# Kernel optimization log

Measured on AMD Instinct MI355X. Metric: run time of the kernel, lower is better.

The kernel has to match this reference:

```python
import jax, jax.numpy as jnp
import numpy as np

N_NODES = 50000
N_EDGES = 800000
IN_FEAT = 128
N_HEADS = 4
OUT_FEAT = 16
NEG_SLOPE = 0.2


def setup_inputs() -> dict:
    key = jax.random.key(0)
    k1, k2, k3, k4, k5 = jax.random.split(key, 5)
    x = jax.random.normal(k1, (N_NODES, IN_FEAT), dtype=jnp.float32)
    src = jax.random.randint(k2, (N_EDGES,), 0, N_NODES)
    dst = jax.random.randint(k3, (N_EDGES,), 0, N_NODES)
    edge_index = jnp.stack([src, dst]).astype(jnp.int64)
    # xavier-uniform-like init for params
    limW = np.sqrt(6.0 / (IN_FEAT + N_HEADS * OUT_FEAT))
    W = jax.random.uniform(k4, (IN_FEAT, N_HEADS * OUT_FEAT), minval=-limW, maxval=limW, dtype=jnp.float32)
    lima = np.sqrt(6.0 / (N_HEADS + 2 * OUT_FEAT))
    a = jax.random.uniform(k5, (1, N_HEADS, 2 * OUT_FEAT), minval=-lima, maxval=lima, dtype=jnp.float32)
    return {"x": x, "edge_index": edge_index, "W": W, "a": a}


def reference(x, edge_index, W, a):
    N = x.shape[0]
    H = a.shape[1]
    F = a.shape[2] // 2
    src, dst = edge_index[0], edge_index[1]
    # node projection: [N, H, F]
    h = (x @ W).reshape(N, H, F)
    # split attention vector: sum(a * cat(h_src, h_dst)) = a_src.h_src + a_dst.h_dst
    a_src = a[0, :, :F]  # [H, F]
    a_dst = a[0, :, F:]  # [H, F]
    e_src = jnp.einsum('nhf,hf->nh', h, a_src)  # [N, H]
    e_dst = jnp.einsum('nhf,hf->nh', h, a_dst)  # [N, H]
    edge_e = jax.nn.leaky_relu(e_src[src] + e_dst[dst], NEG_SLOPE)  # [E, H]
    # softmax over heads (dim=1 in the source)
    alpha = jax.nn.softmax(edge_e, axis=1)  # [E, H]
    # dropout is identity in eval mode
    msg = alpha[:, :, None] * h[src]  # [E, H, F]
    out = jax.ops.segment_sum(msg, dst, num_segments=N)  # [N, H, F]
    # concat=True
    return out.reshape(N, H * F)
```

## Files before the change

### kernel.cpp

```cpp
#include <hip/hip_runtime.h>
#include <hip/hip_bf16.h>

#define IN_FEAT 128
#define N_HEADS 4
#define OUT_FEAT 16
#define HF 64
#define NEG_SLOPE 0.2f

#define BSHIFT 7
#define BNODES 128
#define NBUCK_MAX 512
#define NPB 512

typedef __hip_bfloat16 bf16;
typedef __attribute__((ext_vector_type(8))) short short8;
typedef __attribute__((ext_vector_type(4))) float f32x4;

__device__ inline unsigned short f2b(float f) {
  bf16 b = __float2bfloat16(f);
  return *(unsigned short*)&b;
}
__device__ inline float b2f(unsigned short u) {
  return __uint_as_float((unsigned)u << 16);
}

__global__ __launch_bounds__(256) void k_gemm(
    const float* __restrict__ x, const float* __restrict__ W,
    const float* __restrict__ a, unsigned short* __restrict__ h16,
    float* __restrict__ e_src, float* __restrict__ e_dst, int n_nodes) {
  __shared__ unsigned short xs[64][136];
  __shared__ unsigned short wt[64][136];
  __shared__ unsigned short sh[64][68];
  const int t = threadIdx.x;
  const int nb = blockIdx.x * 64;
  const int lane = t & 63;
  const int w = t >> 6;

  const float4* x4 = (const float4*)x;
  for (int i = t; i < 64 * 32; i += 256) {
    int n = i >> 5, k4 = i & 31;
    int gn = nb + n;
    float4 v = (gn < n_nodes) ? x4[(size_t)gn * 32 + k4]
                              : make_float4(0.f, 0.f, 0.f, 0.f);
    ushort4 u;
    u.x = f2b(v.x); u.y = f2b(v.y); u.z = f2b(v.z); u.w = f2b(v.w);
    *(ushort4*)&xs[n][k4 * 4] = u;
  }
  for (int i = t; i < IN_FEAT * HF; i += 256) {
    int k = i >> 6, c = i & 63;
    wt[c][k] = f2b(W[i]);
  }
  __syncthreads();

  const int m = lane & 15;
  const int q = lane >> 4;
  f32x4 acc[4];
#pragma unroll
  for (int nt = 0; nt < 4; ++nt) acc[nt] = (f32x4){0.f, 0.f, 0.f, 0.f};

#pragma unroll
  for (int kc = 0; kc < 4; ++kc) {
    short8 af = *(const short8*)&xs[w * 16 + m][kc * 32 + q * 8];
#pragma unroll
    for (int nt = 0; nt < 4; ++nt) {
      short8 bfr = *(const short8*)&wt[nt * 16 + m][kc * 32 + q * 8];
      acc[nt] = __builtin_amdgcn_mfma_f32_16x16x32_bf16(af, bfr, acc[nt], 0, 0, 0);
    }
  }

#pragma unroll
  for (int nt = 0; nt < 4; ++nt)
#pragma unroll
    for (int r = 0; r < 4; ++r)
      sh[w * 16 + q * 4 + r][nt * 16 + m] = f2b(acc[nt][r]);
  __syncthreads();

  {
    int n = t >> 2, hd = t & 3;
    int gn = nb + n;
    if (gn < n_nodes) {
      float es = 0.f, ed = 0.f;
#pragma unroll
      for (int f = 0; f < OUT_FEAT; ++f) {
        float hv = b2f(sh[n][hd * 16 + f]);
        es = fmaf(hv, a[hd * 2 * OUT_FEAT + f], es);
        ed = fmaf(hv, a[hd * 2 * OUT_FEAT + OUT_FEAT + f], ed);
      }
      e_src[gn * N_HEADS + hd] = es;
      e_dst[gn * N_HEADS + hd] = ed;
    }
  }

  for (int i = t; i < 64 * 16; i += 256) {
    int n = i >> 4, c4 = (i & 15) * 4;
    int gn = nb + n;
    if (gn < n_nodes) {
      ushort4 v;
      v.x = sh[n][c4 + 0]; v.y = sh[n][c4 + 1];
      v.z = sh[n][c4 + 2]; v.w = sh[n][c4 + 3];
      *(ushort4*)(h16 + (size_t)gn * HF + c4) = v;
    }
  }
}

__global__ __launch_bounds__(256) void k_bh(
    const int* __restrict__ dst, int* __restrict__ bh,
    int nbuck, int chunk, int n_edges) {
  __shared__ int h[NBUCK_MAX];
  int t = threadIdx.x;
  for (int k = t; k < NBUCK_MAX; k += 256) h[k] = 0;
  __syncthreads();
  int beg = blockIdx.x * chunk;
  int end = min(beg + chunk, n_edges);
  for (int e = beg + t; e < end; e += 256)
    atomicAdd(&h[dst[e] >> BSHIFT], 1);
  __syncthreads();
  for (int k = t; k < nbuck; k += 256)
    bh[(size_t)k * NPB + blockIdx.x] = h[k];
}

__global__ __launch_bounds__(NPB) void k_scanA(
    const int* __restrict__ bh, int* __restrict__ sbase, int* __restrict__ tot) {
  __shared__ int s[NPB];
  int t = threadIdx.x, k = blockIdx.x;
  int v = bh[(size_t)k * NPB + t];
  s[t] = v;
  __syncthreads();
  for (int off = 1; off < NPB; off <<= 1) {
    int u = (t >= off) ? s[t - off] : 0;
    __syncthreads();
    s[t] += u;
    __syncthreads();
  }
  sbase[(size_t)k * NPB + t] = s[t] - v;
  if (t == NPB - 1) tot[k] = s[t];
}

__global__ __launch_bounds__(NPB) void k_scanB(
    const int* __restrict__ tot, int* __restrict__ bucket_base,
    int* __restrict__ offsets, int nbuck, int n_edges, int n_nodes) {
  __shared__ int s[NPB];
  int t = threadIdx.x;
  int v = (t < nbuck) ? tot[t] : 0;
  s[t] = v;
  __syncthreads();
  for (int off = 1; off < NPB; off <<= 1) {
    int u = (t >= off) ? s[t - off] : 0;
    __syncthreads();
    s[t] += u;
    __syncthreads();
  }
  if (t < nbuck) bucket_base[t] = s[t] - v;
  if (t == 0) {
    bucket_base[nbuck] = n_edges;
    offsets[n_nodes] = n_edges;
  }
}

__global__ __launch_bounds__(256) void k_part(
    const int* __restrict__ src, const int* __restrict__ dst,
    const float* __restrict__ e_src, const float* __restrict__ e_dst,
    const int* __restrict__ bucket_base, const int* __restrict__ sbase,
    uint4* __restrict__ recs, int nbuck, int chunk, int n_edges) {
  __shared__ int cur[NBUCK_MAX];
  int t = threadIdx.x;
  for (int k = t; k < nbuck; k += 256)
    cur[k] = bucket_base[k] + sbase[(size_t)k * NPB + blockIdx.x];
  __syncthreads();
  int beg = blockIdx.x * chunk;
  int end = min(beg + chunk, n_edges);
  for (int e = beg + t; e < end; e += 256) {
    int s = src[e], d = dst[e];
    float4 es = ((const float4*)e_src)[s];
    float4 ed = ((const float4*)e_dst)[d];
    float v0 = es.x + ed.x, v1 = es.y + ed.y, v2 = es.z + ed.z, v3 = es.w + ed.w;
    v0 = (v0 > 0.f) ? v0 : NEG_SLOPE * v0;
    v1 = (v1 > 0.f) ? v1 : NEG_SLOPE * v1;
    v2 = (v2 > 0.f) ? v2 : NEG_SLOPE * v2;
    v3 = (v3 > 0.f) ? v3 : NEG_SLOPE * v3;
    float m = fmaxf(fmaxf(v0, v1), fmaxf(v2, v3));
    float e0 = __expf(v0 - m), e1 = __expf(v1 - m);
    float e2 = __expf(v2 - m), e3 = __expf(v3 - m);
    float inv = 1.f / (e0 + e1 + e2 + e3);
    unsigned lo = (unsigned)f2b(e0 * inv) | ((unsigned)f2b(e1 * inv) << 16);
    unsigned hi = (unsigned)f2b(e2 * inv) | ((unsigned)f2b(e3 * inv) << 16);
    int pos = atomicAdd(&cur[d >> BSHIFT], 1);
    recs[pos] = make_uint4((unsigned)s, (unsigned)(d & (BNODES - 1)), lo, hi);
  }
}

__global__ __launch_bounds__(512) void k_sort(
    const uint4* __restrict__ recs, const int* __restrict__ bucket_base,
    int* __restrict__ sorted_src, unsigned long long* __restrict__ alpha8,
    int* __restrict__ offsets, int nbuck, int n_nodes) {
  __shared__ int hist[BNODES];
  __shared__ int cur[BNODES];
  int t = threadIdx.x, k = blockIdx.x;
  int beg = bucket_base[k];
  int n = bucket_base[k + 1] - beg;
  if (t < BNODES) hist[t] = 0;
  __syncthreads();
  for (int j = t; j < n; j += 512)
    atomicAdd(&hist[recs[beg + j].y], 1);
  __syncthreads();
  int v = (t < BNODES) ? hist[t] : 0;
  for (int off = 1; off < BNODES; off <<= 1) {
    int u = (t < BNODES && t >= off) ? hist[t - off] : 0;
    __syncthreads();
    if (t < BNODES) hist[t] += u;
    __syncthreads();
  }
  if (t < BNODES) {
    int pos = beg + hist[t] - v;
    cur[t] = pos;
    int node = (k << BSHIFT) + t;
    if (node < n_nodes) offsets[node] = pos;
  }
  __syncthreads();
  for (int j = t; j < n; j += 512) {
    uint4 r = recs[beg + j];
    int p = atomicAdd(&cur[r.y], 1);
    sorted_src[p] = (int)r.x;
    alpha8[p] = (unsigned long long)r.z | ((unsigned long long)r.w << 32);
  }
}

__global__ __launch_bounds__(256) void k_gather(
    const int* __restrict__ sorted_src,
    const unsigned long long* __restrict__ alpha8,
    const int* __restrict__ offsets, const unsigned short* __restrict__ h16,
    float* __restrict__ out, int n_nodes) {
  int gid = blockIdx.x * 256 + threadIdx.x;
  int d = gid >> 6;
  int c = gid & 63;
  if (d >= n_nodes) return;
  int beg = offsets[d];
  int end = offsets[d + 1];
  unsigned shamt = (unsigned)(c >> 4) * 16;
  float acc = 0.f;
  int j = beg;
  for (; j + 8 <= end; j += 8) {
    int s[8];
    unsigned long long au[8];
    float hv[8];
#pragma unroll
    for (int k = 0; k < 8; ++k) s[k] = sorted_src[j + k];
#pragma unroll
    for (int k = 0; k < 8; ++k) au[k] = alpha8[j + k];
#pragma unroll
    for (int k = 0; k < 8; ++k) hv[k] = b2f(h16[(size_t)s[k] * HF + c]);
#pragma unroll
    for (int k = 0; k < 8; ++k) {
      float al = __uint_as_float(((unsigned)(au[k] >> shamt)) << 16);
      acc = fmaf(al, hv[k], acc);
    }
  }
  for (; j < end; ++j) {
    int s = sorted_src[j];
    unsigned long long au = alpha8[j];
    float al = __uint_as_float(((unsigned)(au >> shamt)) << 16);
    acc = fmaf(al, b2f(h16[(size_t)s * HF + c]), acc);
  }
  out[(size_t)d * HF + c] = acc;
}

extern "C" void kernel_launch(void* const* d_in, const int* in_sizes, int n_in,
                              void* d_out, int out_size, void* d_ws, size_t ws_size,
                              hipStream_t stream) {
  const float* x = (const float*)d_in[0];
  const int* ei = (const int*)d_in[1];
  const float* W = (const float*)d_in[2];
  const float* a = (const float*)d_in[3];
  float* out = (float*)d_out;

  const int n_nodes = in_sizes[0] / IN_FEAT;
  const int n_edges = in_sizes[1] / 2;
  const int* src = ei;
  const int* dst = ei + n_edges;

  const int nbuck = (n_nodes + BNODES - 1) >> BSHIFT;
  const int chunk = (n_edges + NPB - 1) / NPB;

  char* ws = (char*)d_ws;
  size_t off = 0;
  uint4* recs = (uint4*)(ws + off);        off += (size_t)n_edges * 16;
  unsigned long long* alpha8 = (unsigned long long*)(ws + off); off += (size_t)n_edges * 8;
  unsigned short* h16 = (unsigned short*)(ws + off); off += (size_t)n_nodes * HF * 2;
  int* sorted_src = (int*)(ws + off);      off += (size_t)n_edges * 4;
  float* e_src = (float*)(ws + off);       off += (size_t)n_nodes * N_HEADS * 4;
  float* e_dst = (float*)(ws + off);       off += (size_t)n_nodes * N_HEADS * 4;
  int* bh = (int*)(ws + off);              off += (size_t)NBUCK_MAX * NPB * 4;
  int* sbase = (int*)(ws + off);           off += (size_t)NBUCK_MAX * NPB * 4;
  int* tot = (int*)(ws + off);             off += (size_t)NBUCK_MAX * 4;
  int* bucket_base = (int*)(ws + off);     off += (size_t)(NBUCK_MAX + 1) * 4;
  int* offsets = (int*)(ws + off);         off += ((size_t)n_nodes + 16) * 4;

  k_gemm<<<(n_nodes + 63) / 64, 256, 0, stream>>>(x, W, a, h16, e_src, e_dst, n_nodes);
  k_bh<<<NPB, 256, 0, stream>>>(dst, bh, nbuck, chunk, n_edges);
  k_scanA<<<nbuck, NPB, 0, stream>>>(bh, sbase, tot);
  k_scanB<<<1, NPB, 0, stream>>>(tot, bucket_base, offsets, nbuck, n_edges, n_nodes);
  k_part<<<NPB, 256, 0, stream>>>(src, dst, e_src, e_dst, bucket_base, sbase, recs, nbuck, chunk, n_edges);
  k_sort<<<nbuck, 512, 0, stream>>>(recs, bucket_base, sorted_src, alpha8, offsets, nbuck, n_nodes);
  k_gather<<<((size_t)n_nodes * 64 + 255) / 256, 256, 0, stream>>>(
      sorted_src, alpha8, offsets, h16, out, n_nodes);
}
```

Before: 165.6 us.

## Fuse bucket histogram into GEMM kernel and pack sorted edge records

The destination-bucket histogram is moved into the projection GEMM kernel, removing a separate launch, and the partition count now follows the GEMM grid size. The scan kernel is widened to 1024 threads to match. Sorted source indices and packed alphas are merged into a single 16-byte record so the gather issues one load per edge instead of two. The trade-off is more bytes written and read per edge, a larger per-bucket offset table, and a longer scan.

```diff
diff --git a/kernel.cpp b/kernel.cpp
--- a/kernel.cpp
+++ b/kernel.cpp
@@ -10,7 +10,6 @@
 #define BSHIFT 7
 #define BNODES 128
 #define NBUCK_MAX 512
-#define NPB 512
 
 typedef __hip_bfloat16 bf16;
 typedef __attribute__((ext_vector_type(8))) short short8;
@@ -23,18 +22,27 @@
 __device__ inline float b2f(unsigned short u) {
   return __uint_as_float((unsigned)u << 16);
 }
+__device__ inline float alpha_lane(unsigned lo, unsigned hi, unsigned sel) {
+  unsigned wd = (sel & 2u) ? hi : lo;
+  return __uint_as_float(((wd >> ((sel & 1u) * 16u)) & 0xffffu) << 16);
+}
 
 __global__ __launch_bounds__(256) void k_gemm(
     const float* __restrict__ x, const float* __restrict__ W,
     const float* __restrict__ a, unsigned short* __restrict__ h16,
-    float* __restrict__ e_src, float* __restrict__ e_dst, int n_nodes) {
+    float* __restrict__ e_src, float* __restrict__ e_dst,
+    const int* __restrict__ dst, int* __restrict__ bh,
+    int n_nodes, int n_edges, int nbuck, int chunkE, int gb) {
   __shared__ unsigned short xs[64][136];
   __shared__ unsigned short wt[64][136];
   __shared__ unsigned short sh[64][68];
+  __shared__ int bhist[NBUCK_MAX];
   const int t = threadIdx.x;
   const int nb = blockIdx.x * 64;
   const int lane = t & 63;
   const int w = t >> 6;
+
+  for (int i = t; i < NBUCK_MAX; i += 256) bhist[i] = 0;
 
   const float4* x4 = (const float4*)x;
   for (int i = t; i < 64 * 32; i += 256) {
@@ -101,50 +109,45 @@
       *(ushort4*)(h16 + (size_t)gn * HF + c4) = v;
     }
   }
-}
-
-__global__ __launch_bounds__(256) void k_bh(
-    const int* __restrict__ dst, int* __restrict__ bh,
-    int nbuck, int chunk, int n_edges) {
-  __shared__ int h[NBUCK_MAX];
-  int t = threadIdx.x;
-  for (int k = t; k < NBUCK_MAX; k += 256) h[k] = 0;
-  __syncthreads();
-  int beg = blockIdx.x * chunk;
-  int end = min(beg + chunk, n_edges);
-  for (int e = beg + t; e < end; e += 256)
-    atomicAdd(&h[dst[e] >> BSHIFT], 1);
-  __syncthreads();
-  for (int k = t; k < nbuck; k += 256)
-    bh[(size_t)k * NPB + blockIdx.x] = h[k];
-}
-
-__global__ __launch_bounds__(NPB) void k_scanA(
-    const int* __restrict__ bh, int* __restrict__ sbase, int* __restrict__ tot) {
-  __shared__ int s[NPB];
+
+  {
+    int ebeg = blockIdx.x * chunkE;
+    int eend = min(ebeg + chunkE, n_edges);
+    for (int e = ebeg + t; e < eend; e += 256)
+      atomicAdd(&bhist[dst[e] >> BSHIFT], 1);
+    __syncthreads();
+    for (int k = t; k < nbuck; k += 256)
+      bh[(size_t)k * gb + blockIdx.x] = bhist[k];
+  }
+}
+
+__global__ __launch_bounds__(1024) void k_scanA(
+    const int* __restrict__ bh, int* __restrict__ sbase, int* __restrict__ tot,
+    int gb) {
+  __shared__ int s[1024];
   int t = threadIdx.x, k = blockIdx.x;
-  int v = bh[(size_t)k * NPB + t];
+  int v = (t < gb) ? bh[(size_t)k * gb + t] : 0;
   s[t] = v;
   __syncthreads();
-  for (int off = 1; off < NPB; off <<= 1) {
+  for (int off = 1; off < 1024; off <<= 1) {
     int u = (t >= off) ? s[t - off] : 0;
     __syncthreads();
     s[t] += u;
     __syncthreads();
   }
-  sbase[(size_t)k * NPB + t] = s[t] - v;
-  if (t == NPB - 1) tot[k] = s[t];
-}
-
-__global__ __launch_bounds__(NPB) void k_scanB(
+  if (t < gb) sbase[(size_t)k * gb + t] = s[t] - v;
+  if (t == 1023) tot[k] = s[t];
+}
+
+__global__ __launch_bounds__(512) void k_scanB(
     const int* __restrict__ tot, int* __restrict__ bucket_base,
     int* __restrict__ offsets, int nbuck, int n_edges, int n_nodes) {
-  __shared__ int s[NPB];
+  __shared__ int s[512];
   int t = threadIdx.x;
   int v = (t < nbuck) ? tot[t] : 0;
   s[t] = v;
   __syncthreads();
-  for (int off = 1; off < NPB; off <<= 1) {
+  for (int off = 1; off < 512; off <<= 1) {
     int u = (t >= off) ? s[t - off] : 0;
     __syncthreads();
     s[t] += u;
@@ -161,14 +164,14 @@
     const int* __restrict__ src, const int* __restrict__ dst,
     const float* __restrict__ e_src, const float* __restrict__ e_dst,
     const int* __restrict__ bucket_base, const int* __restrict__ sbase,
-    uint4* __restrict__ recs, int nbuck, int chunk, int n_edges) {
+    uint4* __restrict__ recs, int nbuck, int chunkE, int n_edges, int gb) {
   __shared__ int cur[NBUCK_MAX];
   int t = threadIdx.x;
   for (int k = t; k < nbuck; k += 256)
-    cur[k] = bucket_base[k] + sbase[(size_t)k * NPB + blockIdx.x];
-  __syncthreads();
-  int beg = blockIdx.x * chunk;
-  int end = min(beg + chunk, n_edges);
+    cur[k] = bucket_base[k] + sbase[(size_t)k * gb + blockIdx.x];
+  __syncthreads();
+  int beg = blockIdx.x * chunkE;
+  int end = min(beg + chunkE, n_edges);
   for (int e = beg + t; e < end; e += 256) {
     int s = src[e], d = dst[e];
     float4 es = ((const float4*)e_src)[s];
@@ -191,8 +194,8 @@
 
 __global__ __launch_bounds__(512) void k_sort(
     const uint4* __restrict__ recs, const int* __restrict__ bucket_base,
-    int* __restrict__ sorted_src, unsigned long long* __restrict__ alpha8,
-    int* __restrict__ offsets, int nbuck, int n_nodes) {
+    uint4* __restrict__ sorted16, int* __restrict__ offsets,
+    int nbuck, int n_nodes) {
   __shared__ int hist[BNODES];
   __shared__ int cur[BNODES];
   int t = threadIdx.x, k = blockIdx.x;
@@ -220,46 +223,37 @@
   for (int j = t; j < n; j += 512) {
     uint4 r = recs[beg + j];
     int p = atomicAdd(&cur[r.y], 1);
-    sorted_src[p] = (int)r.x;
-    alpha8[p] = (unsigned long long)r.z | ((unsigned long long)r.w << 32);
+    sorted16[p] = make_uint4(r.x, 0u, r.z, r.w);
   }
 }
 
 __global__ __launch_bounds__(256) void k_gather(
-    const int* __restrict__ sorted_src,
-    const unsigned long long* __restrict__ alpha8,
-    const int* __restrict__ offsets, const unsigned short* __restrict__ h16,
-    float* __restrict__ out, int n_nodes) {
+    const uint4* __restrict__ sorted16, const int* __restrict__ offsets,
+    const unsigned short* __restrict__ h16, float* __restrict__ out,
+    int n_nodes) {
   int gid = blockIdx.x * 256 + threadIdx.x;
   int d = gid >> 6;
   int c = gid & 63;
   if (d >= n_nodes) return;
   int beg = offsets[d];
   int end = offsets[d + 1];
-  unsigned shamt = (unsigned)(c >> 4) * 16;
+  unsigned sel = (unsigned)(c >> 4);
   float acc = 0.f;
   int j = beg;
   for (; j + 8 <= end; j += 8) {
-    int s[8];
-    unsigned long long au[8];
+    uint4 r[8];
     float hv[8];
 #pragma unroll
-    for (int k = 0; k < 8; ++k) s[k] = sorted_src[j + k];
-#pragma unroll
-    for (int k = 0; k < 8; ++k) au[k] = alpha8[j + k];
-#pragma unroll
-    for (int k = 0; k < 8; ++k) hv[k] = b2f(h16[(size_t)s[k] * HF + c]);
-#pragma unroll
-    for (int k = 0; k < 8; ++k) {
-      float al = __uint_as_float(((unsigned)(au[k] >> shamt)) << 16);
-      acc = fmaf(al, hv[k], acc);
-    }
+    for (int k = 0; k < 8; ++k) r[k] = sorted16[j + k];
+#pragma unroll
+    for (int k = 0; k < 8; ++k) hv[k] = b2f(h16[(size_t)r[k].x * HF + c]);
+#pragma unroll
+    for (int k = 0; k < 8; ++k)
+      acc = fmaf(alpha_lane(r[k].z, r[k].w, sel), hv[k], acc);
   }
   for (; j < end; ++j) {
-    int s = sorted_src[j];
-    unsigned long long au = alpha8[j];
-    float al = __uint_as_float(((unsigned)(au >> shamt)) << 16);
-    acc = fmaf(al, b2f(h16[(size_t)s * HF + c]), acc);
+    uint4 r = sorted16[j];
+    acc = fmaf(alpha_lane(r.z, r.w, sel), b2f(h16[(size_t)r.x * HF + c]), acc);
   }
   out[(size_t)d * HF + c] = acc;
 }
@@ -279,28 +273,29 @@
   const int* dst = ei + n_edges;
 
   const int nbuck = (n_nodes + BNODES - 1) >> BSHIFT;
-  const int chunk = (n_edges + NPB - 1) / NPB;
+  const int gb = (n_nodes + 63) / 64;
+  const int chunkE = (n_edges + gb - 1) / gb;
 
   char* ws = (char*)d_ws;
   size_t off = 0;
   uint4* recs = (uint4*)(ws + off);        off += (size_t)n_edges * 16;
-  unsigned long long* alpha8 = (unsigned long long*)(ws + off); off += (size_t)n_edges * 8;
+  uint4* sorted16 = (uint4*)(ws + off);    off += (size_t)n_edges * 16;
   unsigned short* h16 = (unsigned short*)(ws + off); off += (size_t)n_nodes * HF * 2;
-  int* sorted_src = (int*)(ws + off);      off += (size_t)n_edges * 4;
   float* e_src = (float*)(ws + off);       off += (size_t)n_nodes * N_HEADS * 4;
   float* e_dst = (float*)(ws + off);       off += (size_t)n_nodes * N_HEADS * 4;
-  int* bh = (int*)(ws + off);              off += (size_t)NBUCK_MAX * NPB * 4;
-  int* sbase = (int*)(ws + off);           off += (size_t)NBUCK_MAX * NPB * 4;
+  int* bh = (int*)(ws + off);              off += (size_t)NBUCK_MAX * gb * 4;
+  int* sbase = (int*)(ws + off);           off += (size_t)NBUCK_MAX * gb * 4;
   int* tot = (int*)(ws + off);             off += (size_t)NBUCK_MAX * 4;
   int* bucket_base = (int*)(ws + off);     off += (size_t)(NBUCK_MAX + 1) * 4;
   int* offsets = (int*)(ws + off);         off += ((size_t)n_nodes + 16) * 4;
 
-  k_gemm<<<(n_nodes + 63) / 64, 256, 0, stream>>>(x, W, a, h16, e_src, e_dst, n_nodes);
-  k_bh<<<NPB, 256, 0, stream>>>(dst, bh, nbuck, chunk, n_edges);
-  k_scanA<<<nbuck, NPB, 0, stream>>>(bh, sbase, tot);
-  k_scanB<<<1, NPB, 0, stream>>>(tot, bucket_base, offsets, nbuck, n_edges, n_nodes);
-  k_part<<<NPB, 256, 0, stream>>>(src, dst, e_src, e_dst, bucket_base, sbase, recs, nbuck, chunk, n_edges);
-  k_sort<<<nbuck, 512, 0, stream>>>(recs, bucket_base, sorted_src, alpha8, offsets, nbuck, n_nodes);
+  k_gemm<<<gb, 256, 0, stream>>>(x, W, a, h16, e_src, e_dst, dst, bh,
+                                 n_nodes, n_edges, nbuck, chunkE, gb);
+  k_scanA<<<nbuck, 1024, 0, stream>>>(bh, sbase, tot, gb);
+  k_scanB<<<1, 512, 0, stream>>>(tot, bucket_base, offsets, nbuck, n_edges, n_nodes);
+  k_part<<<gb, 256, 0, stream>>>(src, dst, e_src, e_dst, bucket_base, sbase,
+                                 recs, nbuck, chunkE, n_edges, gb);
+  k_sort<<<nbuck, 512, 0, stream>>>(recs, bucket_base, sorted16, offsets, nbuck, n_nodes);
   k_gather<<<((size_t)n_nodes * 64 + 255) / 256, 256, 0, stream>>>(
-      sorted_src, alpha8, offsets, h16, out, n_nodes);
-}
+      sorted16, offsets, h16, out, n_nodes);
+}
```

New measurement: 170.3 us. 1.03x slower.
